# Kernel tuning notes

Measured on AMD Instinct MI355X. Metric: run time of the kernel, lower is better.

Reference implementation:

```python
import jax, jax.numpy as jnp
import numpy as np

N_NODES = 160_000
N_EDGES = 640_000
N_GRAPHS = 8_000
IN_FEATS = 74
HID = 63
MAX_DEG = 10
PRED_HID = 128
PRED_DIM = 256
BN_EPS = 1e-5
N_LAYERS = 3
PARAM_NAMES = ['W0', 'b0', 'gamma0', 'beta0', 'W1', 'b1', 'gamma1', 'beta1', 'W2', 'b2', 'gamma2', 'beta2', 'W_ng', 'b_ng', 'W_tr', 'b_tr']


def setup_inputs() -> dict:
    key = jax.random.key(0)
    ks = jax.random.split(key, 20)
    inp = {}
    inp['feats'] = jax.random.normal(ks[0], (N_NODES, IN_FEATS), dtype=jnp.float32)
    inp['src'] = jax.random.randint(ks[1], (N_EDGES,), 0, N_NODES, dtype=jnp.int32)
    inp['dst'] = jax.random.randint(ks[2], (N_EDGES,), 0, N_NODES, dtype=jnp.int32)
    # sorted graph membership: 20 nodes per graph (batched molecular graphs)
    inp['graph_ids'] = jnp.repeat(jnp.arange(N_GRAPHS, dtype=jnp.int32), N_NODES // N_GRAPHS)
    dims = [IN_FEATS, HID, HID, HID]
    for l in range(N_LAYERS):
        fi, fo = dims[l], dims[l + 1]
        inp[f'W{l}'] = jax.random.normal(ks[3 + l], (MAX_DEG, fi, fo), dtype=jnp.float32) / np.float32(np.sqrt(fi))
        inp[f'b{l}'] = jnp.zeros((MAX_DEG, fo), dtype=jnp.float32)
        inp[f'gamma{l}'] = jnp.ones((fo,), dtype=jnp.float32)
        inp[f'beta{l}'] = jnp.zeros((fo,), dtype=jnp.float32)
    inp['W_ng'] = jax.random.normal(ks[10], (HID, PRED_HID), dtype=jnp.float32) / np.float32(np.sqrt(HID))
    inp['b_ng'] = jnp.zeros((PRED_HID,), dtype=jnp.float32)
    inp['W_tr'] = jax.random.normal(ks[11], (2 * PRED_HID, PRED_DIM), dtype=jnp.float32) / np.float32(np.sqrt(2 * PRED_HID))
    inp['b_tr'] = jnp.zeros((PRED_DIM,), dtype=jnp.float32)
    return inp


def _nf_layer(h, src, dst, deg_idx, W, b, gamma, beta):
    # message passing: sum of neighbor features via copy_u / fn.sum
    neigh = jax.ops.segment_sum(h[src], dst, num_segments=N_NODES)
    tot = h + neigh  # self + neighbor sum (Duvenaud neural fingerprint)
    # degree-bucketed linear: compute all MAX_DEG transforms, select per node by degree
    z_all = jnp.einsum('ni,kio->nko', tot, W) + b  # [N, MAX_DEG, out]
    z = jnp.take_along_axis(z_all, deg_idx[:, None, None], axis=1)[:, 0, :]  # [N, out]
    z = jax.nn.relu(z)
    # batchnorm over nodes (training-mode batch statistics, eps=1e-5)
    mu = jnp.mean(z, axis=0)
    var = jnp.var(z, axis=0)
    return (z - mu) * jax.lax.rsqrt(var + BN_EPS) * gamma + beta


def _forward(feats, src, dst, graph_ids, params):
    # in-degree per node, clamped to [1, MAX_DEG] -> weight bucket index
    deg = jax.ops.segment_sum(jnp.ones((N_EDGES,), jnp.float32), dst, num_segments=N_NODES)
    deg_idx = jnp.clip(deg.astype(jnp.int32), 1, MAX_DEG) - 1
    h = feats
    for l in range(N_LAYERS):
        h = _nf_layer(h, src, dst, deg_idx, params[f'W{l}'], params[f'b{l}'],
                      params[f'gamma{l}'], params[f'beta{l}'])
    # node_to_graph linear
    h = h @ params['W_ng'] + params['b_ng']  # [N, PRED_HID]
    # SumAndMax readout over each graph
    g_sum = jax.ops.segment_sum(h, graph_ids, num_segments=N_GRAPHS)
    g_max = jax.ops.segment_max(h, graph_ids, num_segments=N_GRAPHS)
    g = jnp.tanh(jnp.concatenate([g_sum, g_max], axis=-1))  # [G, 2*PRED_HID]
    return g @ params['W_tr'] + params['b_tr']  # [G, PRED_DIM]


def reference(feats, src, dst, graph_ids, W0, b0, gamma0, beta0, W1, b1, gamma1, beta1, W2, b2, gamma2, beta2, W_ng, b_ng, W_tr, b_tr):
    params = dict(zip(PARAM_NAMES, (W0, b0, gamma0, beta0, W1, b1, gamma1, beta1, W2, b2, gamma2, beta2, W_ng, b_ng, W_tr, b_tr)))
    return _forward(feats, src, dst, graph_ids, params)
```

## Files before the change

kernel.cpp:

```cpp
#include <hip/hip_runtime.h>
#include <stdint.h>
#include <math.h>

static constexpr int NN = 160000;
static constexpr int NE = 640000;
static constexpr int NG = 8000;
static constexpr int FH  = 63;
static constexpr int ZST = 64;
static constexpr int FST = 80;
static constexpr int NB  = 64;
static constexpr int LGRID = 2560;

static constexpr size_t OFF_DEGCNT = 0;
static constexpr size_t OFF_CURSOR = 640000;
static constexpr size_t OFF_BCNT   = 1280000;
static constexpr size_t OFF_SPART  = 1280064;
static constexpr size_t ZERO_BYTES = 1673280;
static constexpr size_t OFF_ROWPTR = 1673280;
static constexpr size_t OFF_BLKSUM = 2313472;
static constexpr size_t OFF_COL    = 2315520;
static constexpr size_t OFF_BLIST  = 4875520;
static constexpr size_t OFF_AFC    = 17675520;
static constexpr size_t OFF_BNG2   = 17709312;
static constexpr size_t OFF_PBLK   = 17709824;
static constexpr size_t OFF_FB     = 17710080;
static constexpr size_t OFF_Z0     = 43310080;
static constexpr size_t OFF_Z1     = 63790080;
static constexpr size_t OFF_WNGF   = OFF_Z1;
static constexpr size_t OFF_WTRF   = OFF_Z1 + 32768;

__device__ __forceinline__ float blo(unsigned u) {
    union { unsigned i; float f; } v; v.i = u << 16; return v.f;
}
__device__ __forceinline__ float bhi(unsigned u) {
    union { unsigned i; float f; } v; v.i = u & 0xffff0000u; return v.f;
}
__device__ __forceinline__ unsigned short f2b(float f) {
    union { float f; unsigned i; } v; v.f = f;
    unsigned r = v.i + 0x7fffu + ((v.i >> 16) & 1u);
    return (unsigned short)(r >> 16);
}
__device__ __forceinline__ void acc8(float* a, uint4 q) {
    a[0] += blo(q.x); a[1] += bhi(q.x);
    a[2] += blo(q.y); a[3] += bhi(q.y);
    a[4] += blo(q.z); a[5] += bhi(q.z);
    a[6] += blo(q.w); a[7] += bhi(q.w);
}

typedef __attribute__((ext_vector_type(8))) short bf16x8;
typedef __attribute__((ext_vector_type(4))) float f32x4;
union U8 { uint4 u; bf16x8 b; };

__global__ void k_degree(const int* __restrict__ dst, int* __restrict__ degcnt) {
    int e = blockIdx.x * 256 + threadIdx.x;
    if (e < NE) atomicAdd(&degcnt[dst[e]], 1);
}

__global__ void k_scan1(const int* __restrict__ degcnt, int* __restrict__ row_ptr,
                        int* __restrict__ blksum) {
    __shared__ int s[1024];
    int t = threadIdx.x;
    int i = blockIdx.x * 1024 + t;
    int v = (i < NN) ? degcnt[i] : 0;
    s[t] = v; __syncthreads();
    for (int off = 1; off < 1024; off <<= 1) {
        int x = (t >= off) ? s[t - off] : 0;
        __syncthreads();
        s[t] += x;
        __syncthreads();
    }
    if (i < NN) row_ptr[i + 1] = s[t];
    if (t == 1023) blksum[blockIdx.x] = s[t];
}

__global__ void k_scan2(int* __restrict__ blksum, int nblk) {
    __shared__ int s[256];
    int t = threadIdx.x;
    int v = (t < nblk) ? blksum[t] : 0;
    s[t] = v; __syncthreads();
    for (int off = 1; off < 256; off <<= 1) {
        int x = (t >= off) ? s[t - off] : 0;
        __syncthreads();
        s[t] += x;
        __syncthreads();
    }
    if (t < nblk) blksum[t] = s[t] - v;
}

__global__ void k_scan3(int* __restrict__ row_ptr, const int* __restrict__ blksum) {
    int t = threadIdx.x;
    int i = blockIdx.x * 1024 + t;
    if (i < NN) row_ptr[i + 1] += blksum[blockIdx.x];
    if (i == 0) row_ptr[0] = 0;
}

__global__ void k_cast(const float* __restrict__ feats, unsigned short* __restrict__ fb) {
    int i = blockIdx.x * 256 + threadIdx.x;
    if (i >= NN * FST) return;
    int n = i / FST, c = i - n * FST;
    float v = (c < 74) ? feats[n * 74 + c] : 0.f;
    union { float f; unsigned u; } x; x.f = v;
    unsigned r = x.u + 0x7fffu + ((x.u >> 16) & 1u);
    fb[i] = (unsigned short)(r >> 16);
}

__global__ void __launch_bounds__(1024) k_bucket(
        const int* __restrict__ degcnt, const int* __restrict__ row_ptr,
        int* __restrict__ bcnt, int2* __restrict__ blist) {
    __shared__ int scnt[10], sbase[10];
    int tid = threadIdx.x;
    if (tid < 10) scnt[tid] = 0;
    __syncthreads();
    int n = blockIdx.x * 1024 + tid;
    int k = 0, pos = 0;
    bool v = (n < NN);
    int rp = 0;
    if (v) {
        int d = degcnt[n];
        rp = row_ptr[n];
        k = (d < 1) ? 0 : ((d > 10) ? 9 : d - 1);
        pos = atomicAdd(&scnt[k], 1);
    }
    __syncthreads();
    if (tid < 10) sbase[tid] = scnt[tid] ? atomicAdd(&bcnt[tid], scnt[tid]) : 0;
    __syncthreads();
    if (v) blist[k * NN + sbase[k] + pos] = make_int2(n, rp);
}

__global__ void k_prep(const int* __restrict__ bcnt, int* __restrict__ pblk) {
    if (threadIdx.x == 0) {
        int s = 0; pblk[0] = 0;
        for (int k = 0; k < 10; ++k) { s += (bcnt[k] + NB - 1) / NB; pblk[k + 1] = s; }
    }
}

__global__ void k_fill(const int* __restrict__ src, const int* __restrict__ dst,
                       const int* __restrict__ row_ptr, int* __restrict__ cursor,
                       int* __restrict__ col) {
    int e = blockIdx.x * 256 + threadIdx.x;
    if (e >= NE) return;
    int d = dst[e];
    int pos = row_ptr[d] + atomicAdd(&cursor[d], 1);
    col[pos] = src[e];
}

template<int FI, int IST, bool AFF>
__global__ void __launch_bounds__(256, 2) k_layer(
    const unsigned short* __restrict__ in,
    const float* __restrict__ aff,
    const int* __restrict__ row_ptr, const int* __restrict__ col,
    const int* __restrict__ bcnt, const int2* __restrict__ blist,
    const int* __restrict__ pblk,
    const float* __restrict__ W, const float* __restrict__ B,
    unsigned short* __restrict__ zout, float* __restrict__ spart)
{
    constexpr int CH = IST / 8;
    __shared__ float sW[FI * 63 + 64];
    __shared__ float sTot[4][IST][8];
    __shared__ int   sN[4][8];
    __shared__ float sRed[2][4][64];

    int b = blockIdx.x;
    if (b >= pblk[10]) return;
    int k = 0;
#pragma unroll
    for (int i = 1; i <= 9; ++i) k += (b >= pblk[i]) ? 1 : 0;
    int base = (b - pblk[k]) * NB;
    int cnt = bcnt[k];
    if (base >= cnt) return;

    int tid = threadIdx.x;
    int wave = tid >> 6, lane = tid & 63;
    int t = lane >> 3, r = lane & 7;

    const float* Wk = W + (size_t)k * FI * 63;
#pragma unroll 4
    for (int i = tid; i < FI * 63; i += 256) sW[i] = Wk[i];
    __syncthreads();

    const uint4* inq = (const uint4*)in;
    float bterm = (lane < 63) ? B[k * 63 + lane] : 0.f;
    float lsum = 0.f, lsq = 0.f;

#pragma unroll 1
    for (int it = 0; it < NB / 32; ++it) {
        int idx = base + it * 32 + wave * 8 + t;
        if (base + it * 32 >= cnt) break;
        bool val = (idx < cnt);
        int2 bl = blist[k * NN + (val ? idx : (cnt - 1))];
        int n = bl.x, rs = bl.y;
        int dg = (k >= 1 && k <= 8) ? (k + 1) : (row_ptr[n + 1] - rs);
        if (r == 0) sN[wave][t] = val ? n : -1;

        float a[8] = {0.f, 0.f, 0.f, 0.f, 0.f, 0.f, 0.f, 0.f};
        {
            uint4 q = inq[(size_t)n * CH + r];
            acc8(a, q);
        }
        int d = 0;
#pragma unroll 1
        for (; d + 4 <= dg; d += 4) {
            int c0 = col[rs + d], c1 = col[rs + d + 1];
            int c2 = col[rs + d + 2], c3 = col[rs + d + 3];
            uint4 q0 = inq[(size_t)c0 * CH + r];
            uint4 q1 = inq[(size_t)c1 * CH + r];
            uint4 q2 = inq[(size_t)c2 * CH + r];
            uint4 q3 = inq[(size_t)c3 * CH + r];
            acc8(a, q0); acc8(a, q1); acc8(a, q2); acc8(a, q3);
        }
#pragma unroll 1
        for (; d < dg; ++d) {
            int c = col[rs + d];
            uint4 q = inq[(size_t)c * CH + r];
            acc8(a, q);
        }

        if constexpr (IST == 80) {
            float e2[8] = {0.f, 0.f, 0.f, 0.f, 0.f, 0.f, 0.f, 0.f};
            if (r < 2) {
                uint4 q = inq[(size_t)n * CH + 8 + r];
                acc8(e2, q);
                int d2 = 0;
#pragma unroll 1
                for (; d2 < dg; ++d2) {
                    int c = col[rs + d2];
                    uint4 p = inq[(size_t)c * CH + 8 + r];
                    acc8(e2, p);
                }
#pragma unroll
                for (int j = 0; j < 8; ++j) sTot[wave][64 + 8 * r + j][t] = e2[j];
            }
        }

        if constexpr (AFF) {
            const float4* af = (const float4*)aff;
            float4 A0 = af[2 * r], A1 = af[2 * r + 1];
            float4 C0 = af[16 + 2 * r], C1 = af[16 + 2 * r + 1];
            float dp1 = (float)(dg + 1);
            a[0] = A0.x * a[0] + dp1 * C0.x;  a[1] = A0.y * a[1] + dp1 * C0.y;
            a[2] = A0.z * a[2] + dp1 * C0.z;  a[3] = A0.w * a[3] + dp1 * C0.w;
            a[4] = A1.x * a[4] + dp1 * C1.x;  a[5] = A1.y * a[5] + dp1 * C1.y;
            a[6] = A1.z * a[6] + dp1 * C1.z;  a[7] = A1.w * a[7] + dp1 * C1.w;
        }

#pragma unroll
        for (int j = 0; j < 8; ++j) sTot[wave][8 * r + j][t] = a[j];

        float acc[8];
#pragma unroll
        for (int i = 0; i < 8; ++i) acc[i] = bterm;
#pragma unroll 4
        for (int j = 0; j < FI; ++j) {
            float w = sW[j * 63 + lane];
            float4 u = *(const float4*)&sTot[wave][j][0];
            float4 v = *(const float4*)&sTot[wave][j][4];
            acc[0] = fmaf(u.x, w, acc[0]); acc[1] = fmaf(u.y, w, acc[1]);
            acc[2] = fmaf(u.z, w, acc[2]); acc[3] = fmaf(u.w, w, acc[3]);
            acc[4] = fmaf(v.x, w, acc[4]); acc[5] = fmaf(v.y, w, acc[5]);
            acc[6] = fmaf(v.z, w, acc[6]); acc[7] = fmaf(v.w, w, acc[7]);
        }

#pragma unroll
        for (int tt = 0; tt < 8; ++tt) {
            int nn = sN[wave][tt];
            float z = fmaxf(acc[tt], 0.f);
            if (nn >= 0 && lane < 63) {
                zout[(size_t)nn * ZST + lane] = f2b(z);
                lsum += z; lsq += z * z;
            }
        }
    }

    sRed[0][wave][lane] = lsum;
    sRed[1][wave][lane] = lsq;
    __syncthreads();
    if (wave == 0 && lane < 63) {
        float s = sRed[0][0][lane] + sRed[0][1][lane] + sRed[0][2][lane] + sRed[0][3][lane];
        float q = sRed[1][0][lane] + sRed[1][1][lane] + sRed[1][2][lane] + sRed[1][3][lane];
        float* sp = spart + (size_t)(blockIdx.x & 255) * 128;
        atomicAdd(&sp[lane], s);
        atomicAdd(&sp[64 + lane], q);
    }
}

__global__ void k_bn(const float* __restrict__ spart, const float* __restrict__ gamma,
                     const float* __restrict__ beta, float* __restrict__ afc) {
    int o = threadIdx.x;
    if (o >= 63) return;
    double s = 0.0, q = 0.0;
    for (int cp = 0; cp < 256; ++cp) {
        s += (double)spart[cp * 128 + o];
        q += (double)spart[cp * 128 + 64 + o];
    }
    double mu  = s / NN;
    double var = q / NN - mu * mu;
    float a = (float)((double)gamma[o] / sqrt(var + 1e-5));
    float c = (float)((double)beta[o] - mu * (double)a);
    afc[o] = a;
    afc[64 + o] = c;
}

__global__ void k_prepw(const float* __restrict__ W_ng, const float* __restrict__ b_ng,
                        const float* __restrict__ afc2, const float* __restrict__ W_tr,
                        unsigned short* __restrict__ WngF, unsigned short* __restrict__ WtrF,
                        float* __restrict__ bng2) {
    int bid = blockIdx.x, tid = threadIdx.x;
    if (bid == 0) {
        if (tid < 128) {
            float acc = b_ng[tid];
            for (int j = 0; j < 63; ++j)
                acc = fmaf(afc2[64 + j], W_ng[j * 128 + tid], acc);
            bng2[tid] = acc;
        }
    } else if (bid <= 64) {
        int idx = (bid - 1) * 256 + tid;
        int j = idx & 7, lane = (idx >> 3) & 63;
        int nt = (idx >> 9) & 7, kb = idx >> 12;
        int k = (kb & 1) * 32 + ((lane >> 4) << 3) + j;
        int col = nt * 16 + (lane & 15);
        float w = (k < 63) ? afc2[k] * W_ng[k * 128 + col] : 0.f;
        unsigned short hi = f2b(w);
        if (kb < 2) WngF[idx] = hi;
        else        WngF[idx] = f2b(w - blo(hi));
    } else {
        int idx = (bid - 65) * 256 + tid;
        int j = idx & 7, lane = (idx >> 3) & 63;
        int kb = (idx >> 9) & 7, nt = idx >> 12;
        int k = kb * 32 + ((lane >> 4) << 3) + j;
        int col = nt * 16 + (lane & 15);
        WtrF[idx] = f2b(W_tr[k * 256 + col]);
    }
}

__global__ void __launch_bounds__(256, 2) k_graph(
    const unsigned short* __restrict__ Z2, const unsigned short* __restrict__ WngF,
    const float* __restrict__ bng2, const unsigned short* __restrict__ WtrF,
    const float* __restrict__ b_tr, float* __restrict__ out)
{
    __shared__ unsigned short sW[16384];
    __shared__ float sT[16 * 256];
    __shared__ float sB[128];

    int tid = threadIdx.x;
    int wave = tid >> 6, lane = tid & 63;
    int gl15 = lane & 15, grp = lane >> 4;

    {
        const uint4* srcq = (const uint4*)WngF;
        uint4* dstq = (uint4*)sW;
#pragma unroll
        for (int i = 0; i < 8; ++i) dstq[tid + 256 * i] = srcq[tid + 256 * i];
    }
    if (tid < 128) sB[tid] = bng2[tid];
    __syncthreads();

    int nodeBase = blockIdx.x * 320 + wave * 80;
    const uint4* zq = (const uint4*)Z2;
    uint4 a0[5], a1[5];
#pragma unroll
    for (int m = 0; m < 5; ++m) {
        size_t row = (size_t)(nodeBase + m * 16 + gl15) * 8;
        a0[m] = zq[row + grp];
        a1[m] = zq[row + 4 + grp];
    }
    if (grp == 3) {
#pragma unroll
        for (int m = 0; m < 5; ++m) a1[m].w &= 0xffffu;
    }

    const uint4* swq = (const uint4*)sW;
    const float NEGI = -3.0e38f;

#pragma unroll 1
    for (int nt = 0; nt < 8; ++nt) {
        U8 b0, b1, b2, b3;
        b0.u = swq[(0 * 8 + nt) * 64 + lane];
        b1.u = swq[(1 * 8 + nt) * 64 + lane];
        b2.u = swq[(2 * 8 + nt) * 64 + lane];
        b3.u = swq[(3 * 8 + nt) * 64 + lane];

        f32x4 ac[5];
#pragma unroll
        for (int m = 0; m < 5; ++m) {
            U8 xa0, xa1; xa0.u = a0[m]; xa1.u = a1[m];
            f32x4 c = {0.f, 0.f, 0.f, 0.f};
            c = __builtin_amdgcn_mfma_f32_16x16x32_bf16(xa0.b, b0.b, c, 0, 0, 0);
            c = __builtin_amdgcn_mfma_f32_16x16x32_bf16(xa1.b, b1.b, c, 0, 0, 0);
            c = __builtin_amdgcn_mfma_f32_16x16x32_bf16(xa0.b, b2.b, c, 0, 0, 0);
            c = __builtin_amdgcn_mfma_f32_16x16x32_bf16(xa1.b, b3.b, c, 0, 0, 0);
            ac[m] = c;
        }

        float s[4] = {0.f, 0.f, 0.f, 0.f};
        float x[4] = {NEGI, NEGI, NEGI, NEGI};
        bool cA = lane < 16, cB = lane < 32, cC = lane < 48;
#pragma unroll
        for (int r = 0; r < 4; ++r) {
            float v0 = ac[0][r]; s[0] += v0; x[0] = fmaxf(x[0], v0);
            float v4 = ac[4][r]; s[3] += v4; x[3] = fmaxf(x[3], v4);
            float v1 = ac[1][r]; float v1a = cA ? v1 : 0.f;
            s[0] += v1a; s[1] += v1 - v1a;
            x[0] = fmaxf(x[0], cA ? v1 : NEGI); x[1] = fmaxf(x[1], cA ? NEGI : v1);
            float v2 = ac[2][r]; float v2a = cB ? v2 : 0.f;
            s[1] += v2a; s[2] += v2 - v2a;
            x[1] = fmaxf(x[1], cB ? v2 : NEGI); x[2] = fmaxf(x[2], cB ? NEGI : v2);
            float v3 = ac[3][r]; float v3a = cC ? v3 : 0.f;
            s[2] += v3a; s[3] += v3 - v3a;
            x[2] = fmaxf(x[2], cC ? v3 : NEGI); x[3] = fmaxf(x[3], cC ? NEGI : v3);
        }
#pragma unroll
        for (int g = 0; g < 4; ++g) {
            s[g] += __shfl_xor(s[g], 16);
            s[g] += __shfl_xor(s[g], 32);
            x[g] = fmaxf(x[g], __shfl_xor(x[g], 16));
            x[g] = fmaxf(x[g], __shfl_xor(x[g], 32));
        }
        if (lane < 16) {
            int c = nt * 16 + lane;
            float bb = sB[c];
#pragma unroll
            for (int g = 0; g < 4; ++g) {
                int row = wave * 4 + g;
                int swz = (row & 7) << 2;
                sT[(row * 256 + c) ^ swz]       = tanhf(s[g] + 20.f * bb);
                sT[(row * 256 + 128 + c) ^ swz] = tanhf(x[g] + bb);
            }
        }
    }
    __syncthreads();

    U8 pa[8];
    {
        int swz = (gl15 & 7) << 2;
#pragma unroll
        for (int kb = 0; kb < 8; ++kb) {
            int k8 = kb * 32 + grp * 8;
            float4 t0 = *(const float4*)&sT[(gl15 * 256 + k8) ^ swz];
            float4 t1 = *(const float4*)&sT[(gl15 * 256 + k8 + 4) ^ swz];
            unsigned u0 = (unsigned)f2b(t0.x) | ((unsigned)f2b(t0.y) << 16);
            unsigned u1 = (unsigned)f2b(t0.z) | ((unsigned)f2b(t0.w) << 16);
            unsigned u2 = (unsigned)f2b(t1.x) | ((unsigned)f2b(t1.y) << 16);
            unsigned u3 = (unsigned)f2b(t1.z) | ((unsigned)f2b(t1.w) << 16);
            pa[kb].u = make_uint4(u0, u1, u2, u3);
        }
    }
    const uint4* wtq = (const uint4*)WtrF;
    size_t gbase = (size_t)blockIdx.x * 16 * 256;
#pragma unroll 2
    for (int i = 0; i < 4; ++i) {
        int nt = wave * 4 + i;
        f32x4 c = {0.f, 0.f, 0.f, 0.f};
#pragma unroll
        for (int kb = 0; kb < 8; ++kb) {
            U8 b; b.u = wtq[(nt * 8 + kb) * 64 + lane];
            c = __builtin_amdgcn_mfma_f32_16x16x32_bf16(pa[kb].b, b.b, c, 0, 0, 0);
        }
        int d = nt * 16 + gl15;
        float btv = b_tr[d];
#pragma unroll
        for (int r = 0; r < 4; ++r) {
            int row = grp * 4 + r;
            out[gbase + (size_t)row * 256 + d] = c[r] + btv;
        }
    }
}

extern "C" void kernel_launch(void* const* d_in, const int* in_sizes, int n_in,
                              void* d_out, int out_size, void* d_ws, size_t ws_size,
                              hipStream_t stream) {
    const float* feats = (const float*)d_in[0];
    const int*   src   = (const int*)d_in[1];
    const int*   dst   = (const int*)d_in[2];
    const float* W0 = (const float*)d_in[4];
    const float* b0 = (const float*)d_in[5];
    const float* g0 = (const float*)d_in[6];
    const float* be0 = (const float*)d_in[7];
    const float* W1 = (const float*)d_in[8];
    const float* b1 = (const float*)d_in[9];
    const float* g1 = (const float*)d_in[10];
    const float* be1 = (const float*)d_in[11];
    const float* W2 = (const float*)d_in[12];
    const float* b2 = (const float*)d_in[13];
    const float* g2 = (const float*)d_in[14];
    const float* be2 = (const float*)d_in[15];
    const float* Wng = (const float*)d_in[16];
    const float* bng = (const float*)d_in[17];
    const float* Wtr = (const float*)d_in[18];
    const float* btr = (const float*)d_in[19];
    float* out = (float*)d_out;

    char* ws = (char*)d_ws;
    int*    degcnt  = (int*)(ws + OFF_DEGCNT);
    int*    cursor  = (int*)(ws + OFF_CURSOR);
    int*    bcnt    = (int*)(ws + OFF_BCNT);
    float*  spart   = (float*)(ws + OFF_SPART);
    int*    row_ptr = (int*)(ws + OFF_ROWPTR);
    int*    blksum  = (int*)(ws + OFF_BLKSUM);
    int*    col     = (int*)(ws + OFF_COL);
    int2*   blist   = (int2*)(ws + OFF_BLIST);
    float*  afc     = (float*)(ws + OFF_AFC);
    float*  bng2    = (float*)(ws + OFF_BNG2);
    int*    pblk    = (int*)(ws + OFF_PBLK);
    unsigned short* Fb = (unsigned short*)(ws + OFF_FB);
    unsigned short* Z0 = (unsigned short*)(ws + OFF_Z0);
    unsigned short* Z1 = (unsigned short*)(ws + OFF_Z1);
    unsigned short* Z2 = Z0;
    unsigned short* WngF = (unsigned short*)(ws + OFF_WNGF);
    unsigned short* WtrF = (unsigned short*)(ws + OFF_WTRF);

    hipMemsetAsync(d_ws, 0, ZERO_BYTES, stream);

    k_degree<<<NE / 256, 256, 0, stream>>>(dst, degcnt);
    k_cast<<<NN * FST / 256, 256, 0, stream>>>(feats, Fb);
    k_scan1<<<157, 1024, 0, stream>>>(degcnt, row_ptr, blksum);
    k_scan2<<<1, 256, 0, stream>>>(blksum, 157);
    k_scan3<<<157, 1024, 0, stream>>>(row_ptr, blksum);
    k_bucket<<<157, 1024, 0, stream>>>(degcnt, row_ptr, bcnt, blist);
    k_prep<<<1, 64, 0, stream>>>(bcnt, pblk);
    k_fill<<<NE / 256, 256, 0, stream>>>(src, dst, row_ptr, cursor, col);

    k_layer<74, FST, false><<<LGRID, 256, 0, stream>>>(
        Fb, nullptr, row_ptr, col, bcnt, blist, pblk, W0, b0, Z0, spart);
    k_bn<<<1, 64, 0, stream>>>(spart, g0, be0, afc);
    k_layer<63, ZST, true><<<LGRID, 256, 0, stream>>>(
        Z0, afc, row_ptr, col, bcnt, blist, pblk, W1, b1, Z1, spart + 256 * 128);
    k_bn<<<1, 64, 0, stream>>>(spart + 256 * 128, g1, be1, afc + 128);
    k_layer<63, ZST, true><<<LGRID, 256, 0, stream>>>(
        Z1, afc + 128, row_ptr, col, bcnt, blist, pblk, W2, b2, Z2, spart + 2 * 256 * 128);
    k_bn<<<1, 64, 0, stream>>>(spart + 2 * 256 * 128, g2, be2, afc + 256);

    k_prepw<<<321, 256, 0, stream>>>(Wng, bng, afc + 256, Wtr, WngF, WtrF, bng2);
    k_graph<<<NG / 16, 256, 0, stream>>>(Z2, WngF, bng2, WtrF, btr, out);
}
```

Measured before the change: 440.6 us.

## Fold degree count, bucket prep and batchnorm finalize into neighbouring kernels

The degree-count atomics move into the cast kernel, and the standalone k_degree launch is removed. The block-offset prep becomes a last-block epilogue of k_bucket, using an atomic counter and threadfence. The per-layer batchnorm statistics kernel becomes a last-block epilogue of k_layer that reduces the partial sums in double precision across four waves. This removes five small serial launches and their gaps, in exchange for grid-wide completion counters and reuse of the cursor workspace as double scratch.

```diff
diff --git a/kernel.cpp b/kernel.cpp
--- a/kernel.cpp
+++ b/kernel.cpp
@@ -51,9 +51,16 @@
 typedef __attribute__((ext_vector_type(4))) float f32x4;
 union U8 { uint4 u; bf16x8 b; };
 
-__global__ void k_degree(const int* __restrict__ dst, int* __restrict__ degcnt) {
-    int e = blockIdx.x * 256 + threadIdx.x;
-    if (e < NE) atomicAdd(&degcnt[dst[e]], 1);
+__global__ void k_cast(const float* __restrict__ feats, unsigned short* __restrict__ fb,
+                       const int* __restrict__ dst, int* __restrict__ degcnt) {
+    int i = blockIdx.x * 256 + threadIdx.x;
+    if (i < NE) atomicAdd(&degcnt[dst[i]], 1);
+    if (i >= NN * FST) return;
+    int n = i / FST, c = i - n * FST;
+    float v = (c < 74) ? feats[n * 74 + c] : 0.f;
+    union { float f; unsigned u; } x; x.f = v;
+    unsigned r = x.u + 0x7fffu + ((x.u >> 16) & 1u);
+    fb[i] = (unsigned short)(r >> 16);
 }
 
 __global__ void k_scan1(const int* __restrict__ degcnt, int* __restrict__ row_ptr,
@@ -94,20 +101,12 @@
     if (i == 0) row_ptr[0] = 0;
 }
 
-__global__ void k_cast(const float* __restrict__ feats, unsigned short* __restrict__ fb) {
-    int i = blockIdx.x * 256 + threadIdx.x;
-    if (i >= NN * FST) return;
-    int n = i / FST, c = i - n * FST;
-    float v = (c < 74) ? feats[n * 74 + c] : 0.f;
-    union { float f; unsigned u; } x; x.f = v;
-    unsigned r = x.u + 0x7fffu + ((x.u >> 16) & 1u);
-    fb[i] = (unsigned short)(r >> 16);
-}
-
 __global__ void __launch_bounds__(1024) k_bucket(
         const int* __restrict__ degcnt, const int* __restrict__ row_ptr,
-        int* __restrict__ bcnt, int2* __restrict__ blist) {
+        int* __restrict__ bcnt, int2* __restrict__ blist,
+        int* __restrict__ pblk, int* __restrict__ ctr) {
     __shared__ int scnt[10], sbase[10];
+    __shared__ int sLast;
     int tid = threadIdx.x;
     if (tid < 10) scnt[tid] = 0;
     __syncthreads();
@@ -125,12 +124,17 @@
     if (tid < 10) sbase[tid] = scnt[tid] ? atomicAdd(&bcnt[tid], scnt[tid]) : 0;
     __syncthreads();
     if (v) blist[k * NN + sbase[k] + pos] = make_int2(n, rp);
-}
-
-__global__ void k_prep(const int* __restrict__ bcnt, int* __restrict__ pblk) {
-    if (threadIdx.x == 0) {
+
+    if (tid == 0) {
+        __threadfence();
+        sLast = (atomicAdd(ctr, 1) == (int)gridDim.x - 1) ? 1 : 0;
+    }
+    __syncthreads();
+    if (sLast && tid == 0) {
+        __threadfence();
+        const volatile int* bc = bcnt;
         int s = 0; pblk[0] = 0;
-        for (int k = 0; k < 10; ++k) { s += (bcnt[k] + NB - 1) / NB; pblk[k + 1] = s; }
+        for (int kk = 0; kk < 10; ++kk) { s += (bc[kk] + NB - 1) / NB; pblk[kk + 1] = s; }
     }
 }
 
@@ -152,152 +156,174 @@
     const int* __restrict__ bcnt, const int2* __restrict__ blist,
     const int* __restrict__ pblk,
     const float* __restrict__ W, const float* __restrict__ B,
-    unsigned short* __restrict__ zout, float* __restrict__ spart)
+    unsigned short* __restrict__ zout, float* __restrict__ spart,
+    const float* __restrict__ gamma, const float* __restrict__ beta,
+    float* __restrict__ afcOut, int* __restrict__ ctr,
+    double* __restrict__ dscr)
 {
     constexpr int CH = IST / 8;
     __shared__ float sW[FI * 63 + 64];
     __shared__ float sTot[4][IST][8];
     __shared__ int   sN[4][8];
     __shared__ float sRed[2][4][64];
+    __shared__ int   sLast;
 
     int b = blockIdx.x;
-    if (b >= pblk[10]) return;
-    int k = 0;
-#pragma unroll
-    for (int i = 1; i <= 9; ++i) k += (b >= pblk[i]) ? 1 : 0;
-    int base = (b - pblk[k]) * NB;
-    int cnt = bcnt[k];
-    if (base >= cnt) return;
-
     int tid = threadIdx.x;
     int wave = tid >> 6, lane = tid & 63;
     int t = lane >> 3, r = lane & 7;
 
-    const float* Wk = W + (size_t)k * FI * 63;
+    bool work = (b < pblk[10]);
+    int k = 0, base = 0, cnt = 0;
+    if (work) {
+#pragma unroll
+        for (int i = 1; i <= 9; ++i) k += (b >= pblk[i]) ? 1 : 0;
+        base = (b - pblk[k]) * NB;
+        cnt = bcnt[k];
+        if (base >= cnt) work = false;
+    }
+
+    if (work) {
+        const float* Wk = W + (size_t)k * FI * 63;
 #pragma unroll 4
-    for (int i = tid; i < FI * 63; i += 256) sW[i] = Wk[i];
-    __syncthreads();
-
-    const uint4* inq = (const uint4*)in;
-    float bterm = (lane < 63) ? B[k * 63 + lane] : 0.f;
-    float lsum = 0.f, lsq = 0.f;
+        for (int i = tid; i < FI * 63; i += 256) sW[i] = Wk[i];
+        __syncthreads();
+
+        const uint4* inq = (const uint4*)in;
+        float bterm = (lane < 63) ? B[k * 63 + lane] : 0.f;
+        float lsum = 0.f, lsq = 0.f;
 
 #pragma unroll 1
-    for (int it = 0; it < NB / 32; ++it) {
-        int idx = base + it * 32 + wave * 8 + t;
-        if (base + it * 32 >= cnt) break;
-        bool val = (idx < cnt);
-        int2 bl = blist[k * NN + (val ? idx : (cnt - 1))];
-        int n = bl.x, rs = bl.y;
-        int dg = (k >= 1 && k <= 8) ? (k + 1) : (row_ptr[n + 1] - rs);
-        if (r == 0) sN[wave][t] = val ? n : -1;
-
-        float a[8] = {0.f, 0.f, 0.f, 0.f, 0.f, 0.f, 0.f, 0.f};
-        {
-            uint4 q = inq[(size_t)n * CH + r];
-            acc8(a, q);
-        }
-        int d = 0;
+        for (int it = 0; it < NB / 32; ++it) {
+            int idx = base + it * 32 + wave * 8 + t;
+            if (base + it * 32 >= cnt) break;
+            bool val = (idx < cnt);
+            int2 bl = blist[k * NN + (val ? idx : (cnt - 1))];
+            int n = bl.x, rs = bl.y;
+            int dg = (k >= 1 && k <= 8) ? (k + 1) : (row_ptr[n + 1] - rs);
+            if (r == 0) sN[wave][t] = val ? n : -1;
+
+            float a[8] = {0.f, 0.f, 0.f, 0.f, 0.f, 0.f, 0.f, 0.f};
+            {
+                uint4 q = inq[(size_t)n * CH + r];
+                acc8(a, q);
+            }
+            int d = 0;
 #pragma unroll 1
-        for (; d + 4 <= dg; d += 4) {
-            int c0 = col[rs + d], c1 = col[rs + d + 1];
-            int c2 = col[rs + d + 2], c3 = col[rs + d + 3];
-            uint4 q0 = inq[(size_t)c0 * CH + r];
-            uint4 q1 = inq[(size_t)c1 * CH + r];
-            uint4 q2 = inq[(size_t)c2 * CH + r];
-            uint4 q3 = inq[(size_t)c3 * CH + r];
-            acc8(a, q0); acc8(a, q1); acc8(a, q2); acc8(a, q3);
-        }
+            for (; d + 4 <= dg; d += 4) {
+                int c0 = col[rs + d], c1 = col[rs + d + 1];
+                int c2 = col[rs + d + 2], c3 = col[rs + d + 3];
+                uint4 q0 = inq[(size_t)c0 * CH + r];
+                uint4 q1 = inq[(size_t)c1 * CH + r];
+                uint4 q2 = inq[(size_t)c2 * CH + r];
+                uint4 q3 = inq[(size_t)c3 * CH + r];
+                acc8(a, q0); acc8(a, q1); acc8(a, q2); acc8(a, q3);
+            }
 #pragma unroll 1
-        for (; d < dg; ++d) {
-            int c = col[rs + d];
-            uint4 q = inq[(size_t)c * CH + r];
-            acc8(a, q);
-        }
-
-        if constexpr (IST == 80) {
-            float e2[8] = {0.f, 0.f, 0.f, 0.f, 0.f, 0.f, 0.f, 0.f};
-            if (r < 2) {
-                uint4 q = inq[(size_t)n * CH + 8 + r];
-                acc8(e2, q);
-                int d2 = 0;
+            for (; d < dg; ++d) {
+                int c = col[rs + d];
+                uint4 q = inq[(size_t)c * CH + r];
+                acc8(a, q);
+            }
+
+            if constexpr (IST == 80) {
+                float e2[8] = {0.f, 0.f, 0.f, 0.f, 0.f, 0.f, 0.f, 0.f};
+                if (r < 2) {
+                    uint4 q = inq[(size_t)n * CH + 8 + r];
+                    acc8(e2, q);
+                    int d2 = 0;
 #pragma unroll 1
-                for (; d2 < dg; ++d2) {
-                    int c = col[rs + d2];
-                    uint4 p = inq[(size_t)c * CH + 8 + r];
-                    acc8(e2, p);
+                    for (; d2 < dg; ++d2) {
+                        int c = col[rs + d2];
+                        uint4 p = inq[(size_t)c * CH + 8 + r];
+                        acc8(e2, p);
+                    }
+#pragma unroll
+                    for (int j = 0; j < 8; ++j) sTot[wave][64 + 8 * r + j][t] = e2[j];
                 }
-#pragma unroll
-                for (int j = 0; j < 8; ++j) sTot[wave][64 + 8 * r + j][t] = e2[j];
-            }
-        }
-
-        if constexpr (AFF) {
-            const float4* af = (const float4*)aff;
-            float4 A0 = af[2 * r], A1 = af[2 * r + 1];
-            float4 C0 = af[16 + 2 * r], C1 = af[16 + 2 * r + 1];
-            float dp1 = (float)(dg + 1);
-            a[0] = A0.x * a[0] + dp1 * C0.x;  a[1] = A0.y * a[1] + dp1 * C0.y;
-            a[2] = A0.z * a[2] + dp1 * C0.z;  a[3] = A0.w * a[3] + dp1 * C0.w;
-            a[4] = A1.x * a[4] + dp1 * C1.x;  a[5] = A1.y * a[5] + dp1 * C1.y;
-            a[6] = A1.z * a[6] + dp1 * C1.z;  a[7] = A1.w * a[7] + dp1 * C1.w;
-        }
-
-#pragma unroll
-        for (int j = 0; j < 8; ++j) sTot[wave][8 * r + j][t] = a[j];
-
-        float acc[8];
-#pragma unroll
-        for (int i = 0; i < 8; ++i) acc[i] = bterm;
+            }
+
+            if constexpr (AFF) {
+                const float4* af = (const float4*)aff;
+                float4 A0 = af[2 * r], A1 = af[2 * r + 1];
+                float4 C0 = af[16 + 2 * r], C1 = af[16 + 2 * r + 1];
+                float dp1 = (float)(dg + 1);
+                a[0] = A0.x * a[0] + dp1 * C0.x;  a[1] = A0.y * a[1] + dp1 * C0.y;
+                a[2] = A0.z * a[2] + dp1 * C0.z;  a[3] = A0.w * a[3] + dp1 * C0.w;
+                a[4] = A1.x * a[4] + dp1 * C1.x;  a[5] = A1.y * a[5] + dp1 * C1.y;
+                a[6] = A1.z * a[6] + dp1 * C1.z;  a[7] = A1.w * a[7] + dp1 * C1.w;
+            }
+
+#pragma unroll
+            for (int j = 0; j < 8; ++j) sTot[wave][8 * r + j][t] = a[j];
+
+            float acc[8];
+#pragma unroll
+            for (int i = 0; i < 8; ++i) acc[i] = bterm;
 #pragma unroll 4
-        for (int j = 0; j < FI; ++j) {
-            float w = sW[j * 63 + lane];
-            float4 u = *(const float4*)&sTot[wave][j][0];
-            float4 v = *(const float4*)&sTot[wave][j][4];
-            acc[0] = fmaf(u.x, w, acc[0]); acc[1] = fmaf(u.y, w, acc[1]);
-            acc[2] = fmaf(u.z, w, acc[2]); acc[3] = fmaf(u.w, w, acc[3]);
-            acc[4] = fmaf(v.x, w, acc[4]); acc[5] = fmaf(v.y, w, acc[5]);
-            acc[6] = fmaf(v.z, w, acc[6]); acc[7] = fmaf(v.w, w, acc[7]);
-        }
-
-#pragma unroll
-        for (int tt = 0; tt < 8; ++tt) {
-            int nn = sN[wave][tt];
-            float z = fmaxf(acc[tt], 0.f);
-            if (nn >= 0 && lane < 63) {
-                zout[(size_t)nn * ZST + lane] = f2b(z);
-                lsum += z; lsq += z * z;
-            }
-        }
-    }
-
-    sRed[0][wave][lane] = lsum;
-    sRed[1][wave][lane] = lsq;
-    __syncthreads();
-    if (wave == 0 && lane < 63) {
-        float s = sRed[0][0][lane] + sRed[0][1][lane] + sRed[0][2][lane] + sRed[0][3][lane];
-        float q = sRed[1][0][lane] + sRed[1][1][lane] + sRed[1][2][lane] + sRed[1][3][lane];
-        float* sp = spart + (size_t)(blockIdx.x & 255) * 128;
-        atomicAdd(&sp[lane], s);
-        atomicAdd(&sp[64 + lane], q);
-    }
-}
-
-__global__ void k_bn(const float* __restrict__ spart, const float* __restrict__ gamma,
-                     const float* __restrict__ beta, float* __restrict__ afc) {
-    int o = threadIdx.x;
-    if (o >= 63) return;
-    double s = 0.0, q = 0.0;
-    for (int cp = 0; cp < 256; ++cp) {
-        s += (double)spart[cp * 128 + o];
-        q += (double)spart[cp * 128 + 64 + o];
-    }
-    double mu  = s / NN;
-    double var = q / NN - mu * mu;
-    float a = (float)((double)gamma[o] / sqrt(var + 1e-5));
-    float c = (float)((double)beta[o] - mu * (double)a);
-    afc[o] = a;
-    afc[64 + o] = c;
+            for (int j = 0; j < FI; ++j) {
+                float w = sW[j * 63 + lane];
+                float4 u = *(const float4*)&sTot[wave][j][0];
+                float4 v = *(const float4*)&sTot[wave][j][4];
+                acc[0] = fmaf(u.x, w, acc[0]); acc[1] = fmaf(u.y, w, acc[1]);
+                acc[2] = fmaf(u.z, w, acc[2]); acc[3] = fmaf(u.w, w, acc[3]);
+                acc[4] = fmaf(v.x, w, acc[4]); acc[5] = fmaf(v.y, w, acc[5]);
+                acc[6] = fmaf(v.z, w, acc[6]); acc[7] = fmaf(v.w, w, acc[7]);
+            }
+
+#pragma unroll
+            for (int tt = 0; tt < 8; ++tt) {
+                int nn = sN[wave][tt];
+                float z = fmaxf(acc[tt], 0.f);
+                if (nn >= 0 && lane < 63) {
+                    zout[(size_t)nn * ZST + lane] = f2b(z);
+                    lsum += z; lsq += z * z;
+                }
+            }
+        }
+
+        sRed[0][wave][lane] = lsum;
+        sRed[1][wave][lane] = lsq;
+        __syncthreads();
+        if (wave == 0 && lane < 63) {
+            float s = sRed[0][0][lane] + sRed[0][1][lane] + sRed[0][2][lane] + sRed[0][3][lane];
+            float q = sRed[1][0][lane] + sRed[1][1][lane] + sRed[1][2][lane] + sRed[1][3][lane];
+            float* sp = spart + (size_t)(blockIdx.x & 255) * 128;
+            atomicAdd(&sp[lane], s);
+            atomicAdd(&sp[64 + lane], q);
+        }
+    }
+
+    if (tid == 0) {
+        __threadfence();
+        sLast = (atomicAdd(ctr, 1) == (int)gridDim.x - 1) ? 1 : 0;
+    }
+    __syncthreads();
+    if (sLast) {
+        __threadfence();
+        int o = tid & 63, part = tid >> 6;
+        const volatile float* sp = spart;
+        double s = 0.0, q = 0.0;
+        int cp0 = part * 64;
+#pragma unroll 4
+        for (int cp = cp0; cp < cp0 + 64; ++cp) {
+            s += (double)sp[cp * 128 + o];
+            q += (double)sp[cp * 128 + 64 + o];
+        }
+        dscr[part * 128 + o] = s;
+        dscr[part * 128 + 64 + o] = q;
+        __syncthreads();
+        if (tid < 63) {
+            double S = dscr[tid] + dscr[128 + tid] + dscr[256 + tid] + dscr[384 + tid];
+            double Q = dscr[64 + tid] + dscr[192 + tid] + dscr[320 + tid] + dscr[448 + tid];
+            double mu  = S / NN;
+            double var = Q / NN - mu * mu;
+            float a = (float)((double)gamma[tid] / sqrt(var + 1e-5));
+            float c = (float)((double)beta[tid] - mu * (double)a);
+            afcOut[tid] = a;
+            afcOut[64 + tid] = c;
+        }
+    }
 }
 
 __global__ void k_prepw(const float* __restrict__ W_ng, const float* __restrict__ b_ng,
@@ -492,7 +518,9 @@
     char* ws = (char*)d_ws;
     int*    degcnt  = (int*)(ws + OFF_DEGCNT);
     int*    cursor  = (int*)(ws + OFF_CURSOR);
+    double* dscr    = (double*)(ws + OFF_CURSOR);
     int*    bcnt    = (int*)(ws + OFF_BCNT);
+    int*    ctr     = bcnt + 10;
     float*  spart   = (float*)(ws + OFF_SPART);
     int*    row_ptr = (int*)(ws + OFF_ROWPTR);
     int*    blksum  = (int*)(ws + OFF_BLKSUM);
@@ -510,24 +538,22 @@
 
     hipMemsetAsync(d_ws, 0, ZERO_BYTES, stream);
 
-    k_degree<<<NE / 256, 256, 0, stream>>>(dst, degcnt);
-    k_cast<<<NN * FST / 256, 256, 0, stream>>>(feats, Fb);
+    k_cast<<<NN * FST / 256, 256, 0, stream>>>(feats, Fb, dst, degcnt);
     k_scan1<<<157, 1024, 0, stream>>>(degcnt, row_ptr, blksum);
     k_scan2<<<1, 256, 0, stream>>>(blksum, 157);
     k_scan3<<<157, 1024, 0, stream>>>(row_ptr, blksum);
-    k_bucket<<<157, 1024, 0, stream>>>(degcnt, row_ptr, bcnt, blist);
-    k_prep<<<1, 64, 0, stream>>>(bcnt, pblk);
+    k_bucket<<<157, 1024, 0, stream>>>(degcnt, row_ptr, bcnt, blist, pblk, ctr + 3);
     k_fill<<<NE / 256, 256, 0, stream>>>(src, dst, row_ptr, cursor, col);
 
     k_layer<74, FST, false><<<LGRID, 256, 0, stream>>>(
-        Fb, nullptr, row_ptr, col, bcnt, blist, pblk, W0, b0, Z0, spart);
-    k_bn<<<1, 64, 0, stream>>>(spart, g0, be0, afc);
+        Fb, nullptr, row_ptr, col, bcnt, blist, pblk, W0, b0, Z0, spart,
+        g0, be0, afc, ctr + 0, dscr);
     k_layer<63, ZST, true><<<LGRID, 256, 0, stream>>>(
-        Z0, afc, row_ptr, col, bcnt, blist, pblk, W1, b1, Z1, spart + 256 * 128);
-    k_bn<<<1, 64, 0, stream>>>(spart + 256 * 128, g1, be1, afc + 128);
+        Z0, afc, row_ptr, col, bcnt, blist, pblk, W1, b1, Z1, spart + 256 * 128,
+        g1, be1, afc + 128, ctr + 1, dscr);
     k_layer<63, ZST, true><<<LGRID, 256, 0, stream>>>(
-        Z1, afc + 128, row_ptr, col, bcnt, blist, pblk, W2, b2, Z2, spart + 2 * 256 * 128);
-    k_bn<<<1, 64, 0, stream>>>(spart + 2 * 256 * 128, g2, be2, afc + 256);
+        Z1, afc + 128, row_ptr, col, bcnt, blist, pblk, W2, b2, Z2, spart + 2 * 256 * 128,
+        g2, be2, afc + 256, ctr + 2, dscr);
 
     k_prepw<<<321, 256, 0, stream>>>(Wng, bng, afc + 256, Wtr, WngF, WtrF, bng2);
     k_graph<<<NG / 16, 256, 0, stream>>>(Z2, WngF, bng2, WtrF, btr, out);
```

Measured after the change: 708.9 us. 60.9% more time.
